# Kernel tuning notes

Hardware: AMD Instinct MI355X
Metric: run time of the kernel (lower is better)

The kernel has to match this reference:

```python
import jax, jax.numpy as jnp
import numpy as np

W_H = 512
RING_WIDTH = 1
IN_F = 128
OUT_F = 128


def _ring_ids():
    # static ring assignment per pixel, mirrors torch module's self.r / ring_width bins
    ax = np.arange(-W_H / 2, W_H / 2, dtype=np.float64)
    x, y = np.meshgrid(ax, ax, indexing='ij')
    r = np.sqrt(x * x + y * y)
    ring = (r // RING_WIDTH).astype(np.int32).reshape(-1)  # [H*W]
    len_r = int(np.sqrt(2.0) * (W_H / 2)) + 1
    iter_r = len_r // RING_WIDTH + (1 if len_r % RING_WIDTH != 0 else 0)
    return jnp.asarray(ring), iter_r


def setup_inputs() -> dict:
    key = jax.random.key(0)
    ks = jax.random.split(key, 7)
    return {
        'image_re': jax.random.normal(ks[0], (W_H, W_H, IN_F), jnp.float32),
        'image_im': jax.random.normal(ks[1], (W_H, W_H, IN_F), jnp.float32),
        'mask': jax.random.randint(ks[2], (W_H, W_H), 0, 2).astype(jnp.int32),
        'output_re': jnp.zeros((W_H, W_H, OUT_F), jnp.float32),
        'output_im': jnp.zeros((W_H, W_H, OUT_F), jnp.float32),
        'w1_re': jax.random.normal(ks[3], (IN_F, OUT_F), jnp.float32),
        'w1_im': jax.random.normal(ks[4], (IN_F, OUT_F), jnp.float32),
        'w2_re': jax.random.normal(ks[5], (IN_F, OUT_F), jnp.float32),
        'w2_im': jax.random.normal(ks[6], (IN_F, OUT_F), jnp.float32),
    }


def reference(image_re, image_im, mask, output_re, output_im,
              w1_re, w1_im, w2_re, w2_im):
    ring, n_rings = _ring_ids()
    H, _, F_in = image_re.shape
    x_re = image_re.reshape(-1, F_in)  # [N, F_in]
    x_im = image_im.reshape(-1, F_in)
    m = mask.reshape(-1, 1)
    u = (m == 0).astype(x_re.dtype)  # uncorrupted indicator
    c = (m == 1).astype(x_re.dtype)  # corrupted indicator

    # uncor complex matmul (x*u) @ W1, as 4 real GEMMs
    xu_re, xu_im = x_re * u, x_im * u
    mm1_re = xu_re @ w1_re - xu_im @ w1_im
    mm1_im = xu_re @ w1_im + xu_im @ w1_re

    # per-ring mean of mm1 (denominator = full ring size, matching neighbor.shape[0])
    counts = jax.ops.segment_sum(jnp.ones((x_re.shape[0],), x_re.dtype), ring,
                                 num_segments=n_rings)
    denom = jnp.maximum(counts, 1.0)[:, None]
    sum_re = jax.ops.segment_sum(mm1_re, ring, num_segments=n_rings) / denom
    sum_im = jax.ops.segment_sum(mm1_im, ring, num_segments=n_rings) / denom
    sre = sum_re[ring]  # [N, F_out] per-pixel broadcast of its ring mean
    sim = sum_im[ring]

    # cor complex matmul (x*c) @ W2
    xc_re, xc_im = x_re * c, x_im * c
    mm2_re = xc_re @ w2_re - xc_im @ w2_im
    mm2_im = xc_re @ w2_im + xc_im @ w2_re

    out_re = u * (0.5 * (mm1_re + sre)) + c * (mm2_re - sre)
    out_im = u * (0.5 * (mm1_im + sim)) + c * (mm2_im - sim)
    # real/imag stacked on last axis -> [H, H, F_out, 2]
    return jnp.stack([out_re, out_im], axis=-1).reshape(H, H, -1, 2)
```

## Files before the change

### kernel.cpp

```cpp
#include <hip/hip_runtime.h>
#include <hip/hip_bf16.h>
#include <stdint.h>


#define WH 512
#define NPIX (WH * WH)
#define NF 128
#define NRINGS 363
#define SLAB 1664

typedef unsigned short u16;
typedef __attribute__((ext_vector_type(8))) short short8;
typedef __attribute__((ext_vector_type(4))) float floatx4;

__device__ __forceinline__ u16 f2bf(float x) {
    uint32_t u = __float_as_uint(x);
    uint32_t r = (u + 0x7FFFu + ((u >> 16) & 1u)) >> 16;
    return (u16)r;
}
__device__ __forceinline__ uint32_t pk(float a, float b) {
    return (uint32_t)f2bf(a) | ((uint32_t)f2bf(b) << 16);
}
__device__ __forceinline__ short8 negbf(short8 v) {
    union { short8 s; uint32_t u[4]; } x;
    x.s = v;
    x.u[0] ^= 0x80008000u; x.u[1] ^= 0x80008000u;
    x.u[2] ^= 0x80008000u; x.u[3] ^= 0x80008000u;
    return x.s;
}
__device__ __forceinline__ floatx4 mfma16(short8 a, short8 b, floatx4 c) {
    return __builtin_amdgcn_mfma_f32_16x16x32_bf16(a, b, c, 0, 0, 0);
}
__device__ __forceinline__ void dma16(const void* gsrc, void* ldst) {
    __builtin_amdgcn_global_load_lds(
        (const __attribute__((address_space(1))) void*)gsrc,
        (__attribute__((address_space(3))) void*)ldst, 16, 0, 0);
}
__device__ __forceinline__ int ring_of(int p) {
    int i = p >> 9, j = p & 511;
    int x = i - 256, y = j - 256;
    int r2 = x * x + y * y;
    int R = (int)sqrtf((float)r2);
    while ((R + 1) * (R + 1) <= r2) R++;
    while (R * R > r2) R--;
    return R;
}

#define BROW 40
__global__ void k_build_bt(const float* __restrict__ w1r, const float* __restrict__ w1i,
                           const float* __restrict__ w2r, const float* __restrict__ w2i,
                           u16* __restrict__ bt) {
    int n = blockIdx.x, k = threadIdx.x;
    int src = k * NF + n;
    float a1r = w1r[src], a1i = w1i[src], a2r = w2r[src], a2i = w2i[src];
    int kw = k >> 5, kl = k & 31;
    size_t d = (size_t)kw * 20480 + (size_t)n * BROW + kl;
    bt[d + 0 * 5120] = f2bf(a1r - a2r);
    bt[d + 1 * 5120] = f2bf(a2r);
    bt[d + 2 * 5120] = f2bf(a1i - a2i);
    bt[d + 3 * 5120] = f2bf(a2i);
}

__global__ void k_scatter(const int* __restrict__ mask, int* __restrict__ ctr,
                          int* __restrict__ totcnt, int* __restrict__ list)
{
    int p = blockIdx.x * 256 + threadIdx.x;
    int R = ring_of(p);
    atomicAdd(&totcnt[R], 1);
    if (mask[p] == 0) {
        int slot = atomicAdd(&ctr[R], 1);
        list[R * SLAB + slot] = p;
    }
}

__global__ __launch_bounds__(256) void k_xsum(
    const float* __restrict__ xr, const float* __restrict__ xi,
    const int* __restrict__ ctr, const int* __restrict__ list,
    float* __restrict__ xsum)
{
    const int R = blockIdx.x;
    const int nu = ctr[R];
    const int s0 = blockIdx.y * 128;
    if (s0 >= nu) return;
    const int n = min(128, nu - s0);
    __shared__ int sl[128];
    __shared__ float4 red4[256];
    const int t = threadIdx.x;
    if (t < 128) sl[t] = (t < n) ? list[R * SLAB + s0 + t] : 0;
    __syncthreads();
    const float* src = (t & 128) ? xi : xr;
    const int c4 = t & 31;
    const int j = (t >> 5) & 3;
    float4 acc = {0.0f, 0.0f, 0.0f, 0.0f};
#pragma unroll 4
    for (int k = j; k < n; k += 4) {
        int p = sl[k];
        float4 v = *(const float4*)(src + (size_t)p * NF + c4 * 4);
        acc.x += v.x; acc.y += v.y; acc.z += v.z; acc.w += v.w;
    }
    red4[t] = acc;
    __syncthreads();
    if ((t & 96) == 0) {
        float4 a0 = red4[t], a1 = red4[t + 32], a2 = red4[t + 64], a3 = red4[t + 96];
        int base = R * 256 + ((t >> 7) & 1) * 128 + c4 * 4;
        atomicAdd(&xsum[base + 0], a0.x + a1.x + a2.x + a3.x);
        atomicAdd(&xsum[base + 1], a0.y + a1.y + a2.y + a3.y);
        atomicAdd(&xsum[base + 2], a0.z + a1.z + a2.z + a3.z);
        atomicAdd(&xsum[base + 3], a0.w + a1.w + a2.w + a3.w);
    }
}

__global__ __launch_bounds__(256) void k_smean(
    const float* __restrict__ xsum, const int* __restrict__ totcnt,
    const float* __restrict__ w1r, const float* __restrict__ w1i,
    float* __restrict__ smean)
{
    const int R = blockIdx.x;
    const int t = threadIdx.x;
    const int f = t & 127, part = t >> 7;
    __shared__ float sh[256];
    sh[t] = xsum[R * 256 + t];
    __syncthreads();
    float acc = 0.0f;
#pragma unroll 4
    for (int k = 0; k < NF; k++) {
        float ar = sh[k], ai = sh[128 + k];
        float br = w1r[k * NF + f], bi = w1i[k * NF + f];
        acc += part ? (ar * bi + ai * br) : (ar * br - ai * bi);
    }
    float c = (float)totcnt[R];
    c = (c < 1.0f) ? 1.0f : c;
    smean[R * 256 + f * 2 + part] = acc / c;
}

#define LDS_AR 0
#define LDS_AI 5120
#define LDS_B  10240

__global__ __launch_bounds__(256, 2) void k_gemm(
    const float* __restrict__ xr, const float* __restrict__ xi,
    const int* __restrict__ mask, const u16* __restrict__ bt,
    const float* __restrict__ smean, float* __restrict__ out)
{
    __shared__ u16 lds[30720];
    const int t = threadIdx.x;
    const int pbase = blockIdx.x * 128;
    const int w = t >> 6, lane = t & 63;
    const int quad = lane >> 4, l16 = lane & 15;

    floatx4 accRe[2][8], accIm[2][8];
#pragma unroll
    for (int mi = 0; mi < 2; mi++)
#pragma unroll
        for (int ni = 0; ni < 8; ni++) {
            accRe[mi][ni] = (floatx4)0.0f;
            accIm[mi][ni] = (floatx4)0.0f;
        }

    bool uu[2];
    uu[0] = (mask[pbase + w * 32 + l16] == 0);
    uu[1] = (mask[pbase + w * 32 + 16 + l16] == 0);

    const int sr = t >> 1, sh = t & 1;
    const float4* xr4 = (const float4*)(xr + (size_t)(pbase + sr) * NF);
    const float4* xi4 = (const float4*)(xi + (size_t)(pbase + sr) * NF);

    float4 pr[4], pi[4];
    {
        int qb = sh * 4;
        pr[0] = xr4[qb]; pr[1] = xr4[qb + 1]; pr[2] = xr4[qb + 2]; pr[3] = xr4[qb + 3];
        pi[0] = xi4[qb]; pi[1] = xi4[qb + 1]; pi[2] = xi4[qb + 2]; pi[3] = xi4[qb + 3];
    }

    for (int kw = 0; kw < 4; kw++) {
        if (kw) {
            __builtin_amdgcn_s_barrier();
            __builtin_amdgcn_sched_barrier(0);
            asm volatile("" ::: "memory");
        }
        {
            const char* src = (const char*)bt + (size_t)kw * 40960 + w * 10240 + lane * 16;
            u16* dst = &lds[LDS_B + w * 5120];
#pragma unroll
            for (int c = 0; c < 10; c++)
                dma16(src + c * 1024, dst + c * 512);
        }
        asm volatile("s_waitcnt vmcnt(10)" ::: "memory");
        {
            uint4 a, b;
            a.x = pk(pr[0].x, pr[0].y); a.y = pk(pr[0].z, pr[0].w);
            a.z = pk(pr[1].x, pr[1].y); a.w = pk(pr[1].z, pr[1].w);
            b.x = pk(pr[2].x, pr[2].y); b.y = pk(pr[2].z, pr[2].w);
            b.z = pk(pr[3].x, pr[3].y); b.w = pk(pr[3].z, pr[3].w);
            *(uint4*)&lds[LDS_AR + sr * BROW + sh * 16]     = a;
            *(uint4*)&lds[LDS_AR + sr * BROW + sh * 16 + 8] = b;
            a.x = pk(pi[0].x, pi[0].y); a.y = pk(pi[0].z, pi[0].w);
            a.z = pk(pi[1].x, pi[1].y); a.w = pk(pi[1].z, pi[1].w);
            b.x = pk(pi[2].x, pi[2].y); b.y = pk(pi[2].z, pi[2].w);
            b.z = pk(pi[3].x, pi[3].y); b.w = pk(pi[3].z, pi[3].w);
            *(uint4*)&lds[LDS_AI + sr * BROW + sh * 16]     = a;
            *(uint4*)&lds[LDS_AI + sr * BROW + sh * 16 + 8] = b;
        }
        asm volatile("s_waitcnt vmcnt(0)" ::: "memory");
        if (kw < 3) {
            int qb = (kw + 1) * 8 + sh * 4;
            pr[0] = xr4[qb]; pr[1] = xr4[qb + 1]; pr[2] = xr4[qb + 2]; pr[3] = xr4[qb + 3];
            pi[0] = xi4[qb]; pi[1] = xi4[qb + 1]; pi[2] = xi4[qb + 2]; pi[3] = xi4[qb + 3];
        }
        asm volatile("s_waitcnt lgkmcnt(0)" ::: "memory");
        __builtin_amdgcn_s_barrier();
        __builtin_amdgcn_sched_barrier(0);
        asm volatile("" ::: "memory");

        short8 ar[2], ai[2], aru[2], aiu[2];
#pragma unroll
        for (int mi = 0; mi < 2; mi++) {
            int r = w * 32 + mi * 16 + l16;
            ar[mi] = *(short8*)&lds[LDS_AR + r * BROW + quad * 8];
            ai[mi] = *(short8*)&lds[LDS_AI + r * BROW + quad * 8];
            aru[mi] = uu[mi] ? ar[mi] : (short8)0;
            aiu[mi] = uu[mi] ? ai[mi] : (short8)0;
        }
#pragma unroll
        for (int ni = 0; ni < 8; ni++) {
            int nrow = ni * 16 + l16;
            short8 bDr = *(short8*)&lds[LDS_B + 0 * 5120 + nrow * BROW + quad * 8];
            short8 b2r = *(short8*)&lds[LDS_B + 1 * 5120 + nrow * BROW + quad * 8];
            short8 bDi = *(short8*)&lds[LDS_B + 2 * 5120 + nrow * BROW + quad * 8];
            short8 b2i = *(short8*)&lds[LDS_B + 3 * 5120 + nrow * BROW + quad * 8];
            short8 bDin = negbf(bDi), b2in = negbf(b2i);
#pragma unroll
            for (int mi = 0; mi < 2; mi++) {
                accRe[mi][ni] = mfma16(aru[mi], bDr,  accRe[mi][ni]);
                accRe[mi][ni] = mfma16(ar[mi],  b2r,  accRe[mi][ni]);
                accRe[mi][ni] = mfma16(aiu[mi], bDin, accRe[mi][ni]);
                accRe[mi][ni] = mfma16(ai[mi],  b2in, accRe[mi][ni]);
                accIm[mi][ni] = mfma16(aru[mi], bDi,  accIm[mi][ni]);
                accIm[mi][ni] = mfma16(ar[mi],  b2i,  accIm[mi][ni]);
                accIm[mi][ni] = mfma16(aiu[mi], bDr,  accIm[mi][ni]);
                accIm[mi][ni] = mfma16(ai[mi],  b2r,  accIm[mi][ni]);
            }
        }
    }

    int  Rp[2][4];
    bool up[2][4];
#pragma unroll
    for (int mi = 0; mi < 2; mi++)
#pragma unroll
        for (int r = 0; r < 4; r++) {
            int p = pbase + w * 32 + mi * 16 + quad * 4 + r;
            Rp[mi][r] = ring_of(p);
            up[mi][r] = (mask[p] == 0);
        }
#pragma unroll
    for (int mi = 0; mi < 2; mi++)
#pragma unroll
        for (int ni = 0; ni < 8; ni++)
#pragma unroll
            for (int r = 0; r < 4; r++) {
                int p = pbase + w * 32 + mi * 16 + quad * 4 + r;
                int f = ni * 16 + l16;
                float2 sv = *(const float2*)(smean + (size_t)Rp[mi][r] * 256 + f * 2);
                float vre = accRe[mi][ni][r];
                float vim = accIm[mi][ni][r];
                float2 o;
                if (up[mi][r]) { o.x = 0.5f * (vre + sv.x); o.y = 0.5f * (vim + sv.y); }
                else           { o.x = vre - sv.x;          o.y = vim - sv.y; }
                *(float2*)(out + (size_t)p * 256 + f * 2) = o;
            }
}

extern "C" void kernel_launch(void* const* d_in, const int* in_sizes, int n_in,
                              void* d_out, int out_size, void* d_ws, size_t ws_size,
                              hipStream_t stream)
{
    const float* xr  = (const float*)d_in[0];
    const float* xi  = (const float*)d_in[1];
    const int*   msk = (const int*)d_in[2];
    const float* w1r = (const float*)d_in[5];
    const float* w1i = (const float*)d_in[6];
    const float* w2r = (const float*)d_in[7];
    const float* w2i = (const float*)d_in[8];
    float* out = (float*)d_out;

    char* wsb = (char*)d_ws;
    float* xsum   = (float*)(wsb + 0);
    float* smean  = (float*)(wsb + 371712);
    int*   ctr    = (int*)(wsb + 743424);
    int*   totcnt = (int*)(wsb + 744960);
    int*   list   = (int*)(wsb + 746496);
    u16*   bt     = (u16*)(wsb + 3162624);

    hipMemsetAsync(d_ws, 0, 746496, stream);
    k_build_bt<<<dim3(128), dim3(128), 0, stream>>>(w1r, w1i, w2r, w2i, bt);
    k_scatter<<<dim3(NPIX / 256), dim3(256), 0, stream>>>(msk, ctr, totcnt, list);
    k_xsum<<<dim3(NRINGS, 13), dim3(256), 0, stream>>>(xr, xi, ctr, list, xsum);
    k_smean<<<dim3(NRINGS), dim3(256), 0, stream>>>(xsum, totcnt, w1r, w1i, smean);
    k_gemm<<<dim3(NPIX / 128), dim3(256), 0, stream>>>(xr, xi, msk, bt, smean, out);
}
```

Baseline: 775.6 us.

## Split GEMM block work across eight waves with one M-tile each

Doubles the k_gemm block from 256 to 512 threads. Each wave now computes a single 16-row M tile instead of two, and the A-tile staging and B DMA work are split over twice as many threads. This halves the accumulator registers per thread, which should allow more resident waves and better latency hiding. In exchange, each B fragment read from LDS is reused across only one M tile instead of two, so LDS read traffic per MFMA doubles.

```diff
diff --git a/kernel.cpp b/kernel.cpp
--- a/kernel.cpp
+++ b/kernel.cpp
@@ -137,7 +137,7 @@
 #define LDS_AI 5120
 #define LDS_B  10240
 
-__global__ __launch_bounds__(256, 2) void k_gemm(
+__global__ __launch_bounds__(512, 2) void k_gemm(
     const float* __restrict__ xr, const float* __restrict__ xi,
     const int* __restrict__ mask, const u16* __restrict__ bt,
     const float* __restrict__ smean, float* __restrict__ out)
@@ -148,28 +148,24 @@
     const int w = t >> 6, lane = t & 63;
     const int quad = lane >> 4, l16 = lane & 15;
 
-    floatx4 accRe[2][8], accIm[2][8];
-#pragma unroll
-    for (int mi = 0; mi < 2; mi++)
-#pragma unroll
-        for (int ni = 0; ni < 8; ni++) {
-            accRe[mi][ni] = (floatx4)0.0f;
-            accIm[mi][ni] = (floatx4)0.0f;
-        }
-
-    bool uu[2];
-    uu[0] = (mask[pbase + w * 32 + l16] == 0);
-    uu[1] = (mask[pbase + w * 32 + 16 + l16] == 0);
-
-    const int sr = t >> 1, sh = t & 1;
+    floatx4 accRe[8], accIm[8];
+#pragma unroll
+    for (int ni = 0; ni < 8; ni++) {
+        accRe[ni] = (floatx4)0.0f;
+        accIm[ni] = (floatx4)0.0f;
+    }
+
+    const bool uu = (mask[pbase + w * 16 + l16] == 0);
+
+    const int sr = t >> 2, sh = t & 3;
     const float4* xr4 = (const float4*)(xr + (size_t)(pbase + sr) * NF);
     const float4* xi4 = (const float4*)(xi + (size_t)(pbase + sr) * NF);
 
-    float4 pr[4], pi[4];
+    float4 pr[2], pi[2];
     {
-        int qb = sh * 4;
-        pr[0] = xr4[qb]; pr[1] = xr4[qb + 1]; pr[2] = xr4[qb + 2]; pr[3] = xr4[qb + 3];
-        pi[0] = xi4[qb]; pi[1] = xi4[qb + 1]; pi[2] = xi4[qb + 2]; pi[3] = xi4[qb + 3];
+        int qb = sh * 2;
+        pr[0] = xr4[qb]; pr[1] = xr4[qb + 1];
+        pi[0] = xi4[qb]; pi[1] = xi4[qb + 1];
     }
 
     for (int kw = 0; kw < 4; kw++) {
@@ -179,47 +175,40 @@
             asm volatile("" ::: "memory");
         }
         {
-            const char* src = (const char*)bt + (size_t)kw * 40960 + w * 10240 + lane * 16;
-            u16* dst = &lds[LDS_B + w * 5120];
-#pragma unroll
-            for (int c = 0; c < 10; c++)
+            const char* src = (const char*)bt + (size_t)kw * 40960 + w * 5120 + lane * 16;
+            u16* dst = &lds[LDS_B + w * 2560];
+#pragma unroll
+            for (int c = 0; c < 5; c++)
                 dma16(src + c * 1024, dst + c * 512);
         }
-        asm volatile("s_waitcnt vmcnt(10)" ::: "memory");
+        asm volatile("s_waitcnt vmcnt(5)" ::: "memory");
         {
-            uint4 a, b;
+            uint4 a;
             a.x = pk(pr[0].x, pr[0].y); a.y = pk(pr[0].z, pr[0].w);
             a.z = pk(pr[1].x, pr[1].y); a.w = pk(pr[1].z, pr[1].w);
-            b.x = pk(pr[2].x, pr[2].y); b.y = pk(pr[2].z, pr[2].w);
-            b.z = pk(pr[3].x, pr[3].y); b.w = pk(pr[3].z, pr[3].w);
-            *(uint4*)&lds[LDS_AR + sr * BROW + sh * 16]     = a;
-            *(uint4*)&lds[LDS_AR + sr * BROW + sh * 16 + 8] = b;
+            *(uint4*)&lds[LDS_AR + sr * BROW + sh * 8] = a;
             a.x = pk(pi[0].x, pi[0].y); a.y = pk(pi[0].z, pi[0].w);
             a.z = pk(pi[1].x, pi[1].y); a.w = pk(pi[1].z, pi[1].w);
-            b.x = pk(pi[2].x, pi[2].y); b.y = pk(pi[2].z, pi[2].w);
-            b.z = pk(pi[3].x, pi[3].y); b.w = pk(pi[3].z, pi[3].w);
-            *(uint4*)&lds[LDS_AI + sr * BROW + sh * 16]     = a;
-            *(uint4*)&lds[LDS_AI + sr * BROW + sh * 16 + 8] = b;
+            *(uint4*)&lds[LDS_AI + sr * BROW + sh * 8] = a;
         }
         asm volatile("s_waitcnt vmcnt(0)" ::: "memory");
         if (kw < 3) {
-            int qb = (kw + 1) * 8 + sh * 4;
-            pr[0] = xr4[qb]; pr[1] = xr4[qb + 1]; pr[2] = xr4[qb + 2]; pr[3] = xr4[qb + 3];
-            pi[0] = xi4[qb]; pi[1] = xi4[qb + 1]; pi[2] = xi4[qb + 2]; pi[3] = xi4[qb + 3];
+            int qb = (kw + 1) * 8 + sh * 2;
+            pr[0] = xr4[qb]; pr[1] = xr4[qb + 1];
+            pi[0] = xi4[qb]; pi[1] = xi4[qb + 1];
         }
         asm volatile("s_waitcnt lgkmcnt(0)" ::: "memory");
         __builtin_amdgcn_s_barrier();
         __builtin_amdgcn_sched_barrier(0);
         asm volatile("" ::: "memory");
 
-        short8 ar[2], ai[2], aru[2], aiu[2];
-#pragma unroll
-        for (int mi = 0; mi < 2; mi++) {
-            int r = w * 32 + mi * 16 + l16;
-            ar[mi] = *(short8*)&lds[LDS_AR + r * BROW + quad * 8];
-            ai[mi] = *(short8*)&lds[LDS_AI + r * BROW + quad * 8];
-            aru[mi] = uu[mi] ? ar[mi] : (short8)0;
-            aiu[mi] = uu[mi] ? ai[mi] : (short8)0;
+        short8 ar, ai, aru, aiu;
+        {
+            int r = w * 16 + l16;
+            ar = *(short8*)&lds[LDS_AR + r * BROW + quad * 8];
+            ai = *(short8*)&lds[LDS_AI + r * BROW + quad * 8];
+            aru = uu ? ar : (short8)0;
+            aiu = uu ? ai : (short8)0;
         }
 #pragma unroll
         for (int ni = 0; ni < 8; ni++) {
@@ -229,46 +218,39 @@
             short8 bDi = *(short8*)&lds[LDS_B + 2 * 5120 + nrow * BROW + quad * 8];
             short8 b2i = *(short8*)&lds[LDS_B + 3 * 5120 + nrow * BROW + quad * 8];
             short8 bDin = negbf(bDi), b2in = negbf(b2i);
-#pragma unroll
-            for (int mi = 0; mi < 2; mi++) {
-                accRe[mi][ni] = mfma16(aru[mi], bDr,  accRe[mi][ni]);
-                accRe[mi][ni] = mfma16(ar[mi],  b2r,  accRe[mi][ni]);
-                accRe[mi][ni] = mfma16(aiu[mi], bDin, accRe[mi][ni]);
-                accRe[mi][ni] = mfma16(ai[mi],  b2in, accRe[mi][ni]);
-                accIm[mi][ni] = mfma16(aru[mi], bDi,  accIm[mi][ni]);
-                accIm[mi][ni] = mfma16(ar[mi],  b2i,  accIm[mi][ni]);
-                accIm[mi][ni] = mfma16(aiu[mi], bDr,  accIm[mi][ni]);
-                accIm[mi][ni] = mfma16(ai[mi],  b2r,  accIm[mi][ni]);
-            }
-        }
-    }
-
-    int  Rp[2][4];
-    bool up[2][4];
-#pragma unroll
-    for (int mi = 0; mi < 2; mi++)
+            accRe[ni] = mfma16(aru, bDr,  accRe[ni]);
+            accRe[ni] = mfma16(ar,  b2r,  accRe[ni]);
+            accRe[ni] = mfma16(aiu, bDin, accRe[ni]);
+            accRe[ni] = mfma16(ai,  b2in, accRe[ni]);
+            accIm[ni] = mfma16(aru, bDi,  accIm[ni]);
+            accIm[ni] = mfma16(ar,  b2i,  accIm[ni]);
+            accIm[ni] = mfma16(aiu, bDr,  accIm[ni]);
+            accIm[ni] = mfma16(ai,  b2r,  accIm[ni]);
+        }
+    }
+
+    int  Rp[4];
+    bool up[4];
+#pragma unroll
+    for (int r = 0; r < 4; r++) {
+        int p = pbase + w * 16 + quad * 4 + r;
+        Rp[r] = ring_of(p);
+        up[r] = (mask[p] == 0);
+    }
+#pragma unroll
+    for (int ni = 0; ni < 8; ni++)
 #pragma unroll
         for (int r = 0; r < 4; r++) {
-            int p = pbase + w * 32 + mi * 16 + quad * 4 + r;
-            Rp[mi][r] = ring_of(p);
-            up[mi][r] = (mask[p] == 0);
-        }
-#pragma unroll
-    for (int mi = 0; mi < 2; mi++)
-#pragma unroll
-        for (int ni = 0; ni < 8; ni++)
-#pragma unroll
-            for (int r = 0; r < 4; r++) {
-                int p = pbase + w * 32 + mi * 16 + quad * 4 + r;
-                int f = ni * 16 + l16;
-                float2 sv = *(const float2*)(smean + (size_t)Rp[mi][r] * 256 + f * 2);
-                float vre = accRe[mi][ni][r];
-                float vim = accIm[mi][ni][r];
-                float2 o;
-                if (up[mi][r]) { o.x = 0.5f * (vre + sv.x); o.y = 0.5f * (vim + sv.y); }
-                else           { o.x = vre - sv.x;          o.y = vim - sv.y; }
-                *(float2*)(out + (size_t)p * 256 + f * 2) = o;
-            }
+            int p = pbase + w * 16 + quad * 4 + r;
+            int f = ni * 16 + l16;
+            float2 sv = *(const float2*)(smean + (size_t)Rp[r] * 256 + f * 2);
+            float vre = accRe[ni][r];
+            float vim = accIm[ni][r];
+            float2 o;
+            if (up[r]) { o.x = 0.5f * (vre + sv.x); o.y = 0.5f * (vim + sv.y); }
+            else       { o.x = vre - sv.x;          o.y = vim - sv.y; }
+            *(float2*)(out + (size_t)p * 256 + f * 2) = o;
+        }
 }
 
 extern "C" void kernel_launch(void* const* d_in, const int* in_sizes, int n_in,
@@ -297,5 +279,5 @@
     k_scatter<<<dim3(NPIX / 256), dim3(256), 0, stream>>>(msk, ctr, totcnt, list);
     k_xsum<<<dim3(NRINGS, 13), dim3(256), 0, stream>>>(xr, xi, ctr, list, xsum);
     k_smean<<<dim3(NRINGS), dim3(256), 0, stream>>>(xsum, totcnt, w1r, w1i, smean);
-    k_gemm<<<dim3(NPIX / 128), dim3(256), 0, stream>>>(xr, xi, msk, bt, smean, out);
-}
+    k_gemm<<<dim3(NPIX / 128), dim3(512), 0, stream>>>(xr, xi, msk, bt, smean, out);
+}
```

New measurement: 794.3 us. 2.4% more time.
